# Performance work log

Measured on AMD Instinct MI355X. Metric: run time of the kernel, lower is better.

The kernel has to match this reference:

```python
import jax, jax.numpy as jnp
import numpy as np
from jax import lax

K = 3          # kernel_size
G = 8          # group count in SIFA
EPS = 1e-5     # BN and GN eps


def _bn(x, g, b, m, v):
    # eval-mode BatchNorm2d over channel dim 1
    scale = (g / jnp.sqrt(v + EPS))[None, :, None, None]
    shift = (b - m * g / jnp.sqrt(v + EPS))[None, :, None, None]
    return x * scale + shift


def setup_inputs() -> dict:
    key = jax.random.key(0)
    ks = jax.random.split(key, 20)
    B, C, H, W, OUP = 8, 64, 128, 128, 128
    CE = C * K * K  # expanded channels = 576
    CG = C // G     # channels per group view = 8
    f32 = jnp.float32
    inp = {
        "x": jax.random.normal(ks[0], (B, C, H, W), f32),
        # depthwise generate conv: groups=C, out=C*K^2 -> OIHW [CE,1,K,K]
        "gen_w": jax.random.normal(ks[1], (CE, 1, K, K), f32) * 0.1,
        "gen_bn_g": jnp.ones((CE,), f32) + 0.1 * jax.random.normal(ks[2], (CE,), f32),
        "gen_bn_b": 0.1 * jax.random.normal(ks[3], (CE,), f32),
        "gen_bn_m": 0.05 * jax.random.normal(ks[4], (CE,), f32),
        "gen_bn_v": jax.random.uniform(ks[5], (CE,), f32, 0.5, 1.5),
        # GroupNorm(num_groups=CG, num_channels=CG) affine params
        "gn_w": jnp.ones((CG,), f32) + 0.1 * jax.random.normal(ks[6], (CG,), f32),
        "gn_b": 0.1 * jax.random.normal(ks[7], (CG,), f32),
        # gating params, shape (1, CG, 1, 1)
        "cweight": 0.1 * jax.random.normal(ks[8], (1, CG, 1, 1), f32),
        "cbias": jnp.ones((1, CG, 1, 1), f32) + 0.1 * jax.random.normal(ks[9], (1, CG, 1, 1), f32),
        "sweight": 0.1 * jax.random.normal(ks[10], (1, CG, 1, 1), f32),
        "sbias": jnp.ones((1, CG, 1, 1), f32) + 0.1 * jax.random.normal(ks[11], (1, CG, 1, 1), f32),
        "weights_add": jnp.asarray(0.5, f32),
        # final Conv: C -> OUP, k=K, s=K, p=0, bias=False + BN + SiLU
        "conv_w": jax.random.normal(ks[12], (OUP, C, K, K), f32) * (1.0 / np.sqrt(C * K * K)),
        "conv_bn_g": jnp.ones((OUP,), f32) + 0.1 * jax.random.normal(ks[13], (OUP,), f32),
        "conv_bn_b": 0.1 * jax.random.normal(ks[14], (OUP,), f32),
        "conv_bn_m": 0.05 * jax.random.normal(ks[15], (OUP,), f32),
        "conv_bn_v": jax.random.uniform(ks[16], (OUP,), f32, 0.5, 1.5),
    }
    return inp


def reference(x, gen_w, gen_bn_g, gen_bn_b, gen_bn_m, gen_bn_v,
              gn_w, gn_b, cweight, cbias, sweight, sbias, weights_add,
              conv_w, conv_bn_g, conv_bn_b, conv_bn_m, conv_bn_v):
    B, C, H, W = x.shape
    # --- generate: depthwise conv (groups=C) + BN + ReLU ---
    y = lax.conv_general_dilated(
        x, gen_w, window_strides=(1, 1), padding=[(K // 2, K // 2)] * 2,
        feature_group_count=C,
        dimension_numbers=("NCHW", "OIHW", "NCHW"))  # [B, C*K*K, H, W]
    y = jax.nn.relu(_bn(y, gen_bn_g, gen_bn_b, gen_bn_m, gen_bn_v))
    # --- rearrange 'b c (n1 n2) h w -> b c (h n1) (w n2)' ---
    y = y.reshape(B, C, K, K, H, W)          # (b, c, n1, n2, h, w)
    y = y.transpose(0, 1, 4, 2, 5, 3)        # (b, c, h, n1, w, n2)
    HK, WK = H * K, W * K
    y = y.reshape(B, C, HK, WK)
    # --- group view: (b*G, C//G, HK, WK) ---
    g = y.reshape(B * G, C // G, HK, WK)
    # channel gate: global avg pool -> affine -> sigmoid
    x_ch = jnp.mean(g, axis=(2, 3), keepdims=True)        # [B*G, CG, 1, 1]
    ch = g * jax.nn.sigmoid(cweight * x_ch + cbias)
    # spatial gate: per-channel GroupNorm (num_groups == num_channels)
    mu = jnp.mean(g, axis=(2, 3), keepdims=True)
    var = jnp.var(g, axis=(2, 3), keepdims=True)
    gnorm = (g - mu) / jnp.sqrt(var + EPS)
    gnorm = gnorm * gn_w[None, :, None, None] + gn_b[None, :, None, None]
    sp = g * jax.nn.sigmoid(sweight * gnorm + sbias)
    out = weights_add * ch + (1.0 - weights_add) * sp
    out = out.reshape(B, C, HK, WK)
    # --- final Conv: k=K, s=K, p=0, no bias + BN + SiLU ---
    z = lax.conv_general_dilated(
        out, conv_w, window_strides=(K, K), padding="VALID",
        dimension_numbers=("NCHW", "OIHW", "NCHW"))       # [B, OUP, H, W]
    z = _bn(z, conv_bn_g, conv_bn_b, conv_bn_m, conv_bn_v)
    return z * jax.nn.sigmoid(z)  # SiLU
```

## Files before the change

### kernel.cpp

```cpp
#include <hip/hip_runtime.h>
#include <math.h>


#define EPSF 1e-5f
typedef _Float16 v8h __attribute__((ext_vector_type(8)));
typedef __fp16 fp16x2 __attribute__((ext_vector_type(2)));
typedef float v4f __attribute__((ext_vector_type(4)));

static constexpr int C_ = 64, HW_ = 16384, W_ = 128;
static constexpr int KB_ = 80;

static constexpr int WS_WFOLD = 0;
static constexpr int WS_SHIFT = 5184;
static constexpr int WS_BIAS  = 5760;
static constexpr int WS_GATE  = 5888;
static constexpr int WS_PART  = 7936;
static constexpr int WS_WH    = 73472;
static constexpr int WS_BIMG  = 114688;
static constexpr size_t BIMG_BATCH_F16 = (size_t)128 * KB_ * 128 * 8;
static constexpr size_t BIMG_BATCH_FLT = BIMG_BATCH_F16 / 2;

__device__ __forceinline__ float sigmf(float v) { return 1.f / (1.f + __expf(-v)); }

__device__ __forceinline__ unsigned int pk_u32(float a, float b) {
    fp16x2 h = __builtin_amdgcn_cvt_pkrtz(a, b);
    return __builtin_bit_cast(unsigned int, h);
}

__global__ __launch_bounds__(256) void k_fold(
    const float* __restrict__ gen_w,
    const float* __restrict__ gg, const float* __restrict__ gb,
    const float* __restrict__ gm, const float* __restrict__ gv,
    const float* __restrict__ conv_w,
    const float* __restrict__ cg, const float* __restrict__ cb,
    const float* __restrict__ cm, const float* __restrict__ cv,
    float* __restrict__ ws)
{
    int idx = blockIdx.x * 256 + threadIdx.x;
    _Float16* Whp = (_Float16*)(ws + WS_WH);
    if (idx < 81920) {
        int kb = idx >> 10, oup = (idx >> 3) & 127, e = idx & 7;
        int grp = kb / 10, r = kb - grp * 10;
        int tp = r / 5, cl = r - tp * 5;
        int cbase = grp * 8 + tp * 4;
        int c = -1, j = 0;
        if (cl < 4) { c = cbase + cl; j = e; }
        else if (e < 4) { c = cbase + e; j = 8; }
        float v = 0.f;
        if (c >= 0) {
            float s = cg[oup] * rsqrtf(cv[oup] + EPSF);
            v = conv_w[(oup * C_ + c) * 9 + j] * s;
        }
        Whp[idx] = (_Float16)v;
    } else if (idx < 87104) {
        int i = idx - 81920; int ce = i / 9;
        float s = gg[ce] * rsqrtf(gv[ce] + EPSF);
        ws[WS_WFOLD + i] = gen_w[i] * s;
    } else if (idx < 87680) {
        int ce = idx - 87104;
        float s = gg[ce] * rsqrtf(gv[ce] + EPSF);
        ws[WS_SHIFT + ce] = gb[ce] - gm[ce] * s;
    } else if (idx < 87808) {
        int oup = idx - 87680;
        float s = cg[oup] * rsqrtf(cv[oup] + EPSF);
        ws[WS_BIAS + oup] = cb[oup] - cm[oup] * s;
    }
}

__global__ __launch_bounds__(256) void k_conv(
    const float* __restrict__ x, float* __restrict__ ws, int b0)
{
    __shared__ float xs[4][18 * 19];
    __shared__ float wfl[4][96];
    __shared__ unsigned short j8l[4][256];
    int bid = blockIdx.x;
    int cq = bid & 15, p = (bid >> 4) & 63, bbl = bid >> 10;
    int b = b0 + bbl;
    int oh0 = (p >> 3) << 4, ow0 = (p & 7) << 4;
    int t = threadIdx.x;

    for (int i = t; i < 1296; i += 256) {
        int ch = i / 324, rr = i - ch * 324;
        int r = rr / 18, cc = rr - r * 18;
        int yy = oh0 + r - 1, xx = ow0 + cc - 1;
        float v = 0.f;
        if (yy >= 0 && yy < 128 && xx >= 0 && xx < 128)
            v = x[(size_t)(b * C_ + cq * 4 + ch) * HW_ + yy * 128 + xx];
        xs[ch][r * 19 + cc] = v;
    }
    for (int i = t; i < 384; i += 256) {
        int ch = i / 96, k = i - ch * 96;
        int c = cq * 4 + ch;
        float v = 0.f;
        if (k < 81) v = ws[WS_WFOLD + c * 81 + k];
        else if (k >= 84 && k < 93) v = ws[WS_SHIFT + c * 9 + (k - 84)];
        wfl[ch][k] = v;
    }
    __syncthreads();

    int w = __builtin_amdgcn_readfirstlane(t >> 6);
    int lane = t & 63, r0 = lane >> 4, col = lane & 15;

    float wv[81], sh9[9];
#pragma unroll
    for (int i = 0; i < 20; ++i) {
        float4 v4 = *(const float4*)&wfl[w][i * 4];
        wv[i * 4] = v4.x; wv[i * 4 + 1] = v4.y; wv[i * 4 + 2] = v4.z; wv[i * 4 + 3] = v4.w;
    }
    wv[80] = wfl[w][80];
#pragma unroll
    for (int i = 0; i < 9; ++i) sh9[i] = wfl[w][84 + i];

    float st0 = 0.f, st1 = 0.f;
    int kbBase = (cq >> 1) * 10 + (cq & 1) * 5;
    int tileBase = ((p >> 3) * 2) * 8 + (p & 7);
    _Float16* Bimg = (_Float16*)(ws + WS_BIMG) + (size_t)bbl * BIMG_BATCH_F16;

#pragma unroll 1
    for (int i = 0; i < 4; ++i) {
        int row16 = r0 + 4 * i;
        float nb[9];
#pragma unroll
        for (int dy = 0; dy < 3; ++dy)
#pragma unroll
            for (int dx = 0; dx < 3; ++dx)
                nb[dy * 3 + dx] = xs[w][(row16 + dy) * 19 + col + dx];
        float uv[9];
#pragma unroll
        for (int j = 0; j < 9; ++j) uv[j] = sh9[j];
#pragma unroll
        for (int k = 0; k < 9; ++k) {
            float xv = nb[k];
#pragma unroll
            for (int j = 0; j < 9; ++j) uv[j] = fmaf(wv[j * 9 + k], xv, uv[j]);
        }
#pragma unroll
        for (int j = 0; j < 9; ++j) {
            float v = fmaxf(uv[j], 0.f);
            uv[j] = v;
            st0 += v;
            st1 = fmaf(v, v, st1);
        }
        int tile = tileBase + (row16 >> 3) * 8;
        int px = (row16 & 7) * 16 + col;
        uint4 oc;
        oc.x = pk_u32(uv[0], uv[1]); oc.y = pk_u32(uv[2], uv[3]);
        oc.z = pk_u32(uv[4], uv[5]); oc.w = pk_u32(uv[6], uv[7]);
        *(uint4*)(Bimg + (size_t)(tile * KB_ + kbBase + w) * 1024 + (size_t)px * 8) = oc;
        _Float16 h8 = (_Float16)uv[8];
        j8l[w][row16 * 16 + col] = __builtin_bit_cast(unsigned short, h8);
    }
    __syncthreads();

    {
        int row16 = t >> 4;
        int tile = tileBase + (row16 >> 3) * 8;
        int px = t & 127;
        uint4 oc;
        oc.x = (unsigned int)j8l[0][t] | ((unsigned int)j8l[1][t] << 16);
        oc.y = (unsigned int)j8l[2][t] | ((unsigned int)j8l[3][t] << 16);
        oc.z = 0u; oc.w = 0u;
        *(uint4*)(Bimg + (size_t)(tile * KB_ + kbBase + 4) * 1024 + (size_t)px * 8) = oc;
    }

#pragma unroll
    for (int off = 32; off > 0; off >>= 1) {
        st0 += __shfl_down(st0, off, 64);
        st1 += __shfl_down(st1, off, 64);
    }
    if (lane == 0) {
        float* part = ws + WS_PART;
        part[(size_t)((b * 16 + cq) * 8 + w * 2) * 64 + p] = st0;
        part[(size_t)((b * 16 + cq) * 8 + w * 2 + 1) * 64 + p] = st1;
    }
}

__global__ __launch_bounds__(256) void k_gate(
    const float* __restrict__ part,
    const float* __restrict__ cwt, const float* __restrict__ cbs,
    const float* __restrict__ swt, const float* __restrict__ sbs,
    const float* __restrict__ gnw, const float* __restrict__ gnb,
    const float* __restrict__ wadd, float4* __restrict__ gate, int b0, int nb)
{
    int i = blockIdx.x * 256 + threadIdx.x;
    if (i >= nb * 64) return;
    int b = b0 + (i >> 6), c = i & 63;
    const float* pp = part + (size_t)((b * 16 + (c >> 2)) * 8 + (c & 3) * 2) * 64;
    float s1 = 0.f, s2 = 0.f;
#pragma unroll
    for (int q = 0; q < 16; ++q) {
        float4 a = *(const float4*)(pp + q * 4);
        float4 d = *(const float4*)(pp + 64 + q * 4);
        s1 += a.x + a.y + a.z + a.w;
        s2 += d.x + d.y + d.z + d.w;
    }
    const float N = 9.f * 16384.f;
    float mean = s1 / N;
    float var = s2 / N - mean * mean;
    float inv = rsqrtf(var + EPSF);
    int cgi = c & 7;
    float wa = wadd[0];
    float cgt = sigmf(cwt[cgi] * mean + cbs[cgi]);
    const float NL2E = -1.44269504f;
    float4 o;
    o.x = wa * cgt;
    o.y = 1.f - wa;
    o.z = NL2E * (swt[cgi] * gnw[cgi] * inv);
    o.w = NL2E * (swt[cgi] * (gnb[cgi] - mean * inv * gnw[cgi]) + sbs[cgi]);
    gate[b * 64 + c] = o;
}

__global__ __launch_bounds__(256, 4) void k_main(
    const float* __restrict__ ws, float* __restrict__ out, int b0)
{
    __shared__ _Float16 Bs[40 * 512];
    int t = threadIdx.x;
    int bid = blockIdx.x;
    int half = bid & 1, tile = (bid >> 1) & 127, bbl = bid >> 8;
    int b = b0 + bbl;
    int oh0 = (tile >> 3) << 3, ow0 = (tile & 7) << 4;

    int w = __builtin_amdgcn_readfirstlane(t >> 6);
    int lane = t & 63, quad = lane >> 4, l15 = lane & 15;

    const _Float16* Wh = (const _Float16*)(ws + WS_WH);
    const _Float16* Bimg = (const _Float16*)(ws + WS_BIMG)
        + (size_t)bbl * BIMG_BATCH_F16 + (size_t)tile * (KB_ * 1024)
        + (size_t)(half * 64 + lane) * 8;
    const float4* gp = (const float4*)(ws + WS_GATE) + b * 64;

    v4f acc[2][4];
#pragma unroll
    for (int a = 0; a < 2; ++a)
#pragma unroll
        for (int bb = 0; bb < 4; ++bb) acc[a][bb] = (v4f)0.f;

#pragma unroll 1
    for (int r = 0; r < 2; ++r) {
        if (r) __syncthreads();
#pragma unroll 2
        for (int i = 0; i < 10; ++i) {
            int kl = i * 4 + w;
            int kb = r * 40 + kl;
            int grp = kb / 10, rr = kb - grp * 10;
            int tp = (rr >= 5) ? 1 : 0, cl = rr - tp * 5;
            int cbase = grp * 8 + tp * 4;
            uint4 cell = *(const uint4*)(Bimg + (size_t)kb * 1024);
            v8h v = __builtin_bit_cast(v8h, cell);
            uint4 oc;
            if (cl < 4) {
                float4 g = gp[cbase + cl];
                float u[8];
#pragma unroll
                for (int e = 0; e < 8; ++e) {
                    float f = (float)v[e];
                    float ex = __builtin_amdgcn_exp2f(fmaf(g.z, f, g.w));
                    u[e] = f * fmaf(g.y, __builtin_amdgcn_rcpf(1.f + ex), g.x);
                }
                oc.x = pk_u32(u[0], u[1]); oc.y = pk_u32(u[2], u[3]);
                oc.z = pk_u32(u[4], u[5]); oc.w = pk_u32(u[6], u[7]);
            } else {
                float4 g0 = gp[cbase], g1 = gp[cbase + 1];
                float4 g2 = gp[cbase + 2], g3 = gp[cbase + 3];
                float u[4];
#pragma unroll
                for (int e = 0; e < 4; ++e) {
                    float f = (float)v[e];
                    float4 g = (e == 0) ? g0 : ((e == 1) ? g1 : ((e == 2) ? g2 : g3));
                    float ex = __builtin_amdgcn_exp2f(fmaf(g.z, f, g.w));
                    u[e] = f * fmaf(g.y, __builtin_amdgcn_rcpf(1.f + ex), g.x);
                }
                oc.x = pk_u32(u[0], u[1]); oc.y = pk_u32(u[2], u[3]);
                oc.z = 0u; oc.w = 0u;
            }
            *(uint4*)(Bs + kl * 512 + lane * 8) = oc;
        }
        __syncthreads();
#pragma unroll
        for (int s = 0; s < 10; ++s) {
            int cglob = r * 40 + s * 4 + quad;
            const _Float16* Ap = Wh + ((size_t)cglob * 128 + w * 32 + l15) * 8;
            v8h A0 = *(const v8h*)(Ap);
            v8h A1 = *(const v8h*)(Ap + 128);
            int klq = s * 4 + quad;
            v8h Bf[4];
#pragma unroll
            for (int bb = 0; bb < 4; ++bb)
                Bf[bb] = *(const v8h*)(Bs + klq * 512 + (bb * 16 + l15) * 8);
#pragma unroll
            for (int bb = 0; bb < 4; ++bb) {
                acc[0][bb] = __builtin_amdgcn_mfma_f32_16x16x32_f16(A0, Bf[bb], acc[0][bb], 0, 0, 0);
                acc[1][bb] = __builtin_amdgcn_mfma_f32_16x16x32_f16(A1, Bf[bb], acc[1][bb], 0, 0, 0);
            }
        }
    }

    size_t ob = (size_t)b * 128 * HW_;
#pragma unroll
    for (int a = 0; a < 2; ++a) {
#pragma unroll
        for (int r2 = 0; r2 < 4; ++r2) {
            int oup = w * 32 + a * 16 + quad * 4 + r2;
            float bo = ws[WS_BIAS + oup];
#pragma unroll
            for (int bb = 0; bb < 4; ++bb) {
                int p2 = half * 64 + bb * 16 + l15;
                int py2 = p2 >> 4, px2 = p2 & 15;
                float z = acc[a][bb][r2] + bo;
                out[ob + (size_t)oup * HW_ + (oh0 + py2) * W_ + ow0 + px2] = z * sigmf(z);
            }
        }
    }
}

extern "C" void kernel_launch(void* const* d_in, const int* in_sizes, int n_in,
                              void* d_out, int out_size, void* d_ws, size_t ws_size,
                              hipStream_t stream)
{
    const float* x      = (const float*)d_in[0];
    const float* gen_w  = (const float*)d_in[1];
    const float* gg     = (const float*)d_in[2];
    const float* gb     = (const float*)d_in[3];
    const float* gm     = (const float*)d_in[4];
    const float* gv     = (const float*)d_in[5];
    const float* gnw    = (const float*)d_in[6];
    const float* gnb    = (const float*)d_in[7];
    const float* cwt    = (const float*)d_in[8];
    const float* cbs    = (const float*)d_in[9];
    const float* swt    = (const float*)d_in[10];
    const float* sbs    = (const float*)d_in[11];
    const float* wadd   = (const float*)d_in[12];
    const float* conv_w = (const float*)d_in[13];
    const float* cg2    = (const float*)d_in[14];
    const float* cb2    = (const float*)d_in[15];
    const float* cm2    = (const float*)d_in[16];
    const float* cv2    = (const float*)d_in[17];
    float* ws  = (float*)d_ws;
    float* out = (float*)d_out;

    size_t avail = ws_size / 4;
    int nb = 1;
    const int cands[4] = {8, 4, 2, 1};
    for (int i = 0; i < 4; ++i) {
        if ((size_t)WS_BIMG + (size_t)cands[i] * BIMG_BATCH_FLT <= avail) { nb = cands[i]; break; }
    }

    k_fold<<<343, 256, 0, stream>>>(gen_w, gg, gb, gm, gv, conv_w, cg2, cb2, cm2, cv2, ws);
    for (int b0 = 0; b0 < 8; b0 += nb) {
        k_conv<<<nb * 1024, 256, 0, stream>>>(x, ws, b0);
        k_gate<<<(nb * 64 + 255) / 256, 256, 0, stream>>>(
            ws + WS_PART, cwt, cbs, swt, sbs, gnw, gnb, wadd,
            (float4*)(ws + WS_GATE), b0, nb);
        k_main<<<nb * 256, 256, 0, stream>>>(ws, out, b0);
    }
}
```

Before: 241.3 us.

## Double-buffer gated B tiles in main GEMM and split expand-conv into register-blocked halves

The main kernel now splits the K dimension into four chunks of 20 kb rows with two LDS buffers. Global loads for the next chunk are issued before the MFMAs on the current chunk, and the gating math and LDS store follow them, which overlaps memory latency with matrix work. The expand kernel computes all four pixel rows at once, in two weight halves (4 and 5 outputs), so each weight register is reused across four pixels and fewer weights stay live at once. The cost is more live registers for prefetched cells and neighborhoods, plus an extra barrier per chunk.

Result: no change. 245.7 us (+1.8%).

```diff
diff --git a/kernel.cpp b/kernel.cpp
--- a/kernel.cpp
+++ b/kernel.cpp
@@ -101,54 +101,102 @@
     int w = __builtin_amdgcn_readfirstlane(t >> 6);
     int lane = t & 63, r0 = lane >> 4, col = lane & 15;
 
-    float wv[81], sh9[9];
-#pragma unroll
-    for (int i = 0; i < 20; ++i) {
-        float4 v4 = *(const float4*)&wfl[w][i * 4];
-        wv[i * 4] = v4.x; wv[i * 4 + 1] = v4.y; wv[i * 4 + 2] = v4.z; wv[i * 4 + 3] = v4.w;
-    }
-    wv[80] = wfl[w][80];
-#pragma unroll
-    for (int i = 0; i < 9; ++i) sh9[i] = wfl[w][84 + i];
+    float nb4[4][9];
+#pragma unroll
+    for (int px = 0; px < 4; ++px)
+#pragma unroll
+        for (int dy = 0; dy < 3; ++dy)
+#pragma unroll
+            for (int dx = 0; dx < 3; ++dx)
+                nb4[px][dy * 3 + dx] = xs[w][(r0 + 4 * px + dy) * 19 + col + dx];
 
     float st0 = 0.f, st1 = 0.f;
+    unsigned int pkx[4], pky[4], pkz[4], pkw[4];
+
+    {
+        float wv[36];
+#pragma unroll
+        for (int i = 0; i < 9; ++i) {
+            float4 v4 = *(const float4*)&wfl[w][i * 4];
+            wv[i * 4] = v4.x; wv[i * 4 + 1] = v4.y; wv[i * 4 + 2] = v4.z; wv[i * 4 + 3] = v4.w;
+        }
+        float uv[4][4];
+#pragma unroll
+        for (int j = 0; j < 4; ++j) {
+            float sj = wfl[w][84 + j];
+#pragma unroll
+            for (int px = 0; px < 4; ++px) uv[px][j] = sj;
+        }
+#pragma unroll
+        for (int k = 0; k < 9; ++k)
+#pragma unroll
+            for (int j = 0; j < 4; ++j) {
+                float ww = wv[j * 9 + k];
+#pragma unroll
+                for (int px = 0; px < 4; ++px)
+                    uv[px][j] = fmaf(ww, nb4[px][k], uv[px][j]);
+            }
+#pragma unroll
+        for (int px = 0; px < 4; ++px) {
+            float u0 = fmaxf(uv[px][0], 0.f), u1 = fmaxf(uv[px][1], 0.f);
+            float u2 = fmaxf(uv[px][2], 0.f), u3 = fmaxf(uv[px][3], 0.f);
+            st0 += u0 + u1 + u2 + u3;
+            st1 = fmaf(u0, u0, st1); st1 = fmaf(u1, u1, st1);
+            st1 = fmaf(u2, u2, st1); st1 = fmaf(u3, u3, st1);
+            pkx[px] = pk_u32(u0, u1); pky[px] = pk_u32(u2, u3);
+        }
+    }
+    {
+        float wv[45];
+#pragma unroll
+        for (int i = 0; i < 11; ++i) {
+            float4 v4 = *(const float4*)&wfl[w][36 + i * 4];
+            wv[i * 4] = v4.x; wv[i * 4 + 1] = v4.y; wv[i * 4 + 2] = v4.z; wv[i * 4 + 3] = v4.w;
+        }
+        wv[44] = wfl[w][80];
+        float uv[4][5];
+#pragma unroll
+        for (int jj = 0; jj < 5; ++jj) {
+            float sj = wfl[w][88 + jj];
+#pragma unroll
+            for (int px = 0; px < 4; ++px) uv[px][jj] = sj;
+        }
+#pragma unroll
+        for (int k = 0; k < 9; ++k)
+#pragma unroll
+            for (int jj = 0; jj < 5; ++jj) {
+                float ww = wv[jj * 9 + k];
+#pragma unroll
+                for (int px = 0; px < 4; ++px)
+                    uv[px][jj] = fmaf(ww, nb4[px][k], uv[px][jj]);
+            }
+#pragma unroll
+        for (int px = 0; px < 4; ++px) {
+            float u4 = fmaxf(uv[px][0], 0.f), u5 = fmaxf(uv[px][1], 0.f);
+            float u6 = fmaxf(uv[px][2], 0.f), u7 = fmaxf(uv[px][3], 0.f);
+            float u8 = fmaxf(uv[px][4], 0.f);
+            st0 += u4 + u5 + u6 + u7 + u8;
+            st1 = fmaf(u4, u4, st1); st1 = fmaf(u5, u5, st1);
+            st1 = fmaf(u6, u6, st1); st1 = fmaf(u7, u7, st1);
+            st1 = fmaf(u8, u8, st1);
+            pkz[px] = pk_u32(u4, u5); pkw[px] = pk_u32(u6, u7);
+            _Float16 h8 = (_Float16)u8;
+            int row16 = r0 + 4 * px;
+            j8l[w][row16 * 16 + col] = __builtin_bit_cast(unsigned short, h8);
+        }
+    }
+
     int kbBase = (cq >> 1) * 10 + (cq & 1) * 5;
     int tileBase = ((p >> 3) * 2) * 8 + (p & 7);
     _Float16* Bimg = (_Float16*)(ws + WS_BIMG) + (size_t)bbl * BIMG_BATCH_F16;
-
-#pragma unroll 1
-    for (int i = 0; i < 4; ++i) {
-        int row16 = r0 + 4 * i;
-        float nb[9];
-#pragma unroll
-        for (int dy = 0; dy < 3; ++dy)
-#pragma unroll
-            for (int dx = 0; dx < 3; ++dx)
-                nb[dy * 3 + dx] = xs[w][(row16 + dy) * 19 + col + dx];
-        float uv[9];
-#pragma unroll
-        for (int j = 0; j < 9; ++j) uv[j] = sh9[j];
-#pragma unroll
-        for (int k = 0; k < 9; ++k) {
-            float xv = nb[k];
-#pragma unroll
-            for (int j = 0; j < 9; ++j) uv[j] = fmaf(wv[j * 9 + k], xv, uv[j]);
-        }
-#pragma unroll
-        for (int j = 0; j < 9; ++j) {
-            float v = fmaxf(uv[j], 0.f);
-            uv[j] = v;
-            st0 += v;
-            st1 = fmaf(v, v, st1);
-        }
+#pragma unroll
+    for (int px = 0; px < 4; ++px) {
+        int row16 = r0 + 4 * px;
         int tile = tileBase + (row16 >> 3) * 8;
-        int px = (row16 & 7) * 16 + col;
+        int pxi = (row16 & 7) * 16 + col;
         uint4 oc;
-        oc.x = pk_u32(uv[0], uv[1]); oc.y = pk_u32(uv[2], uv[3]);
-        oc.z = pk_u32(uv[4], uv[5]); oc.w = pk_u32(uv[6], uv[7]);
-        *(uint4*)(Bimg + (size_t)(tile * KB_ + kbBase + w) * 1024 + (size_t)px * 8) = oc;
-        _Float16 h8 = (_Float16)uv[8];
-        j8l[w][row16 * 16 + col] = __builtin_bit_cast(unsigned short, h8);
+        oc.x = pkx[px]; oc.y = pky[px]; oc.z = pkz[px]; oc.w = pkw[px];
+        *(uint4*)(Bimg + (size_t)(tile * KB_ + kbBase + w) * 1024 + (size_t)pxi * 8) = oc;
     }
     __syncthreads();
 
@@ -213,7 +261,7 @@
 __global__ __launch_bounds__(256, 4) void k_main(
     const float* __restrict__ ws, float* __restrict__ out, int b0)
 {
-    __shared__ _Float16 Bs[40 * 512];
+    __shared__ _Float16 Bs[2][20 * 512];
     int t = threadIdx.x;
     int bid = blockIdx.x;
     int half = bid & 1, tile = (bid >> 1) & 127, bbl = bid >> 8;
@@ -235,63 +283,86 @@
 #pragma unroll
         for (int bb = 0; bb < 4; ++bb) acc[a][bb] = (v4f)0.f;
 
+    auto GATE = [&](int kb, uint4 cell) -> uint4 {
+        int grp = kb / 10, rr = kb - grp * 10;
+        int tp = (rr >= 5) ? 1 : 0, cl = rr - tp * 5;
+        int cbase = grp * 8 + tp * 4;
+        v8h v = __builtin_bit_cast(v8h, cell);
+        uint4 oc;
+        if (cl < 4) {
+            float4 g = gp[cbase + cl];
+            float u[8];
+#pragma unroll
+            for (int e = 0; e < 8; ++e) {
+                float f = (float)v[e];
+                float ex = __builtin_amdgcn_exp2f(fmaf(g.z, f, g.w));
+                u[e] = f * fmaf(g.y, __builtin_amdgcn_rcpf(1.f + ex), g.x);
+            }
+            oc.x = pk_u32(u[0], u[1]); oc.y = pk_u32(u[2], u[3]);
+            oc.z = pk_u32(u[4], u[5]); oc.w = pk_u32(u[6], u[7]);
+        } else {
+            float4 g0 = gp[cbase], g1 = gp[cbase + 1];
+            float4 g2 = gp[cbase + 2], g3 = gp[cbase + 3];
+            float u[4];
+#pragma unroll
+            for (int e = 0; e < 4; ++e) {
+                float f = (float)v[e];
+                float4 g = (e == 0) ? g0 : ((e == 1) ? g1 : ((e == 2) ? g2 : g3));
+                float ex = __builtin_amdgcn_exp2f(fmaf(g.z, f, g.w));
+                u[e] = f * fmaf(g.y, __builtin_amdgcn_rcpf(1.f + ex), g.x);
+            }
+            oc.x = pk_u32(u[0], u[1]); oc.y = pk_u32(u[2], u[3]);
+            oc.z = 0u; oc.w = 0u;
+        }
+        return oc;
+    };
+
+#pragma unroll
+    for (int i = 0; i < 5; ++i) {
+        int kl = i * 4 + w;
+        uint4 cell = *(const uint4*)(Bimg + (size_t)kl * 1024);
+        uint4 oc = GATE(kl, cell);
+        *(uint4*)(&Bs[0][kl * 512 + lane * 8]) = oc;
+    }
+    __syncthreads();
+
 #pragma unroll 1
-    for (int r = 0; r < 2; ++r) {
-        if (r) __syncthreads();
-#pragma unroll 2
-        for (int i = 0; i < 10; ++i) {
-            int kl = i * 4 + w;
-            int kb = r * 40 + kl;
-            int grp = kb / 10, rr = kb - grp * 10;
-            int tp = (rr >= 5) ? 1 : 0, cl = rr - tp * 5;
-            int cbase = grp * 8 + tp * 4;
-            uint4 cell = *(const uint4*)(Bimg + (size_t)kb * 1024);
-            v8h v = __builtin_bit_cast(v8h, cell);
-            uint4 oc;
-            if (cl < 4) {
-                float4 g = gp[cbase + cl];
-                float u[8];
-#pragma unroll
-                for (int e = 0; e < 8; ++e) {
-                    float f = (float)v[e];
-                    float ex = __builtin_amdgcn_exp2f(fmaf(g.z, f, g.w));
-                    u[e] = f * fmaf(g.y, __builtin_amdgcn_rcpf(1.f + ex), g.x);
-                }
-                oc.x = pk_u32(u[0], u[1]); oc.y = pk_u32(u[2], u[3]);
-                oc.z = pk_u32(u[4], u[5]); oc.w = pk_u32(u[6], u[7]);
-            } else {
-                float4 g0 = gp[cbase], g1 = gp[cbase + 1];
-                float4 g2 = gp[cbase + 2], g3 = gp[cbase + 3];
-                float u[4];
-#pragma unroll
-                for (int e = 0; e < 4; ++e) {
-                    float f = (float)v[e];
-                    float4 g = (e == 0) ? g0 : ((e == 1) ? g1 : ((e == 2) ? g2 : g3));
-                    float ex = __builtin_amdgcn_exp2f(fmaf(g.z, f, g.w));
-                    u[e] = f * fmaf(g.y, __builtin_amdgcn_rcpf(1.f + ex), g.x);
-                }
-                oc.x = pk_u32(u[0], u[1]); oc.y = pk_u32(u[2], u[3]);
-                oc.z = 0u; oc.w = 0u;
-            }
-            *(uint4*)(Bs + kl * 512 + lane * 8) = oc;
-        }
-        __syncthreads();
-#pragma unroll
-        for (int s = 0; s < 10; ++s) {
-            int cglob = r * 40 + s * 4 + quad;
+    for (int c = 0; c < 4; ++c) {
+        uint4 cin[5];
+        if (c < 3) {
+#pragma unroll
+            for (int i = 0; i < 5; ++i) {
+                int kb = (c + 1) * 20 + i * 4 + w;
+                cin[i] = *(const uint4*)(Bimg + (size_t)kb * 1024);
+            }
+        }
+        const _Float16* bs = Bs[c & 1];
+#pragma unroll
+        for (int s = 0; s < 5; ++s) {
+            int klq = s * 4 + quad;
+            int cglob = c * 20 + klq;
             const _Float16* Ap = Wh + ((size_t)cglob * 128 + w * 32 + l15) * 8;
             v8h A0 = *(const v8h*)(Ap);
             v8h A1 = *(const v8h*)(Ap + 128);
-            int klq = s * 4 + quad;
             v8h Bf[4];
 #pragma unroll
             for (int bb = 0; bb < 4; ++bb)
-                Bf[bb] = *(const v8h*)(Bs + klq * 512 + (bb * 16 + l15) * 8);
+                Bf[bb] = *(const v8h*)&bs[klq * 512 + (bb * 16 + l15) * 8];
 #pragma unroll
             for (int bb = 0; bb < 4; ++bb) {
                 acc[0][bb] = __builtin_amdgcn_mfma_f32_16x16x32_f16(A0, Bf[bb], acc[0][bb], 0, 0, 0);
                 acc[1][bb] = __builtin_amdgcn_mfma_f32_16x16x32_f16(A1, Bf[bb], acc[1][bb], 0, 0, 0);
             }
+        }
+        if (c < 3) {
+            _Float16* bd = Bs[(c + 1) & 1];
+#pragma unroll
+            for (int i = 0; i < 5; ++i) {
+                int kl = i * 4 + w;
+                uint4 oc = GATE((c + 1) * 20 + kl, cin[i]);
+                *(uint4*)(&bd[kl * 512 + lane * 8]) = oc;
+            }
+            __syncthreads();
         }
     }
 
```
